# Kernel tuning notes

Hardware: AMD Instinct MI355X
Metric: run time of the kernel (lower is better)

## Reference

```python
import jax, jax.numpy as jnp
import numpy as np

# dims: B=32 batch, F=40 max_frames, NB=36 num_boxes, R=512 region size, H=512 hidden
# feat_size D = R + 2H = 1536 ; relation attn input = 2D = 3072

def _soft_attention(feats, hidden, Wf, bf, Wh, bh, wa):
    # feats: (N, L, Din), hidden: (N, H) -> att feat (N, Din), alpha (N, L)
    e = jnp.tanh(feats @ Wf.T + bf + (hidden @ Wh.T + bh)[:, None, :]) @ wa  # (N, L)
    alpha = jax.nn.softmax(e, axis=1)
    att = jnp.einsum('nl,nld->nd', alpha, feats)
    return att, alpha


def setup_inputs() -> dict:
    key = jax.random.key(0)
    ks = jax.random.split(key, 16)
    B, F, NB, R, H = 32, 40, 36, 512, 512
    D = R + 2 * H  # 1536
    s = 0.02
    inp = {
        'i3d_feats': jax.random.normal(ks[0], (B, F, 2 * H), jnp.float32),
        'object_feats': jax.random.normal(ks[1], (B, F, NB, R), jnp.float32),
        'hidden_state': jax.random.normal(ks[2], (B, H), jnp.float32),
        # spatial SoftAttention(R, H, H)
        'Ws_f': jax.random.normal(ks[3], (H, R), jnp.float32) * s,
        'bs_f': jnp.zeros((H,), jnp.float32),
        'Ws_h': jax.random.normal(ks[4], (H, H), jnp.float32) * s,
        'bs_h': jnp.zeros((H,), jnp.float32),
        'was': jax.random.normal(ks[5], (H,), jnp.float32) * s,
        # relation SoftAttention(2D, H, H)
        'Wr_f': jax.random.normal(ks[6], (H, 2 * D), jnp.float32) * s,
        'br_f': jnp.zeros((H,), jnp.float32),
        'Wr_h': jax.random.normal(ks[7], (H, H), jnp.float32) * s,
        'br_h': jnp.zeros((H,), jnp.float32),
        'war': jax.random.normal(ks[8], (H,), jnp.float32) * s,
    }
    return inp


def reference(i3d_feats, object_feats, hidden_state,
              Ws_f, bs_f, Ws_h, bs_h, was,
              Wr_f, br_f, Wr_h, br_h, war):
    B, F, NB, R = object_feats.shape
    # ---- spatial attention over boxes (per frame) ----
    feats = object_feats.reshape(B * F, NB, R)
    hidden_rep = jnp.repeat(hidden_state, F, axis=0)  # == hidden.repeat(1,F).reshape(B*F,-1)
    obj_att, _ = _soft_attention(feats, hidden_rep, Ws_f, bs_f, Ws_h, bs_h, was)
    obj_att = obj_att.reshape(B, F, R)
    feat = jnp.concatenate([obj_att, i3d_feats], axis=-1)  # (B, F, D)
    D = feat.shape[-1]
    # ---- relation attention over all F*F frame pairs ----
    # pairwise[b, i*F + j] = concat(feat[b, j], feat[b, i])  (feat1 varies fast, feat2 slow)
    # Decompose Wr_f @ concat(fj, fi) = Wr1 @ fj + Wr2 @ fi to avoid O(F^2 * 2D) tensor.
    Wr1, Wr2 = Wr_f[:, :D], Wr_f[:, D:]
    p1 = feat @ Wr1.T  # (B, F, H), applied to fast index j
    p2 = feat @ Wr2.T  # (B, F, H), applied to slow index i
    hproj = hidden_state @ Wr_h.T + br_h  # (B, H)
    e = jnp.tanh(p2[:, :, None, :] + p1[:, None, :, :] + (hproj + br_f)[:, None, None, :]) @ war  # (B,F,F) [i,j]
    alpha = jax.nn.softmax(e.reshape(B, F * F), axis=1).reshape(B, F, F)
    # weighted sum of concat(feat[j], feat[i]) splits into two marginal sums
    rel1 = jnp.einsum('bij,bjd->bd', alpha, feat)
    rel2 = jnp.einsum('bij,bid->bd', alpha, feat)
    return jnp.concatenate([rel1, rel2], axis=-1)  # (B, 2D)
```

## Files before the change

kernel.cpp:

```cpp
#include <hip/hip_runtime.h>
#include <stdint.h>

#define B_SZ 32
#define F_SZ 40
#define NB_SZ 36
#define R_SZ 512
#define H_SZ 512
#define D_SZ 1536
#define M1 (B_SZ * F_SZ * NB_SZ)
#define NROW (B_SZ * F_SZ)
#define FNB (F_SZ * NB_SZ)

typedef __attribute__((ext_vector_type(8))) short short8;
typedef __attribute__((ext_vector_type(4))) float f32x4;

__device__ __forceinline__ unsigned short f2bf(float f) {
    unsigned int x = __float_as_uint(f);
    return (unsigned short)((x + 0x7fffu + ((x >> 16) & 1u)) >> 16);
}
__device__ __forceinline__ float bf2f(unsigned short u) {
    union { unsigned int i; float f; } v; v.i = ((unsigned int)u) << 16; return v.f;
}
__device__ __forceinline__ unsigned int cvtpk(float lo, float hi) {
    unsigned int r;
    asm("v_cvt_pk_bf16_f32 %0, %1, %2" : "=v"(r) : "v"(lo), "v"(hi));
    return r;
}
__device__ __forceinline__ float fast_rcp(float x) {
    float r; asm("v_rcp_f32 %0, %1" : "=v"(r) : "v"(x)); return r;
}
__device__ __forceinline__ float fast_tanh(float x) {
    float t = __builtin_amdgcn_exp2f(2.8853900817779268f * x);
    return 1.0f - 2.0f * fast_rcp(t + 1.0f);
}

__device__ __forceinline__ void gload_lds16(const void* gsrc, void* ldst) {
    __builtin_amdgcn_global_load_lds(
        (const __attribute__((address_space(1))) unsigned int*)gsrc,
        (__attribute__((address_space(3))) unsigned int*)ldst, 16, 0, 0);
}

__global__ __launch_bounds__(256) void k_pre(
    const float* __restrict__ hidden,
    const float* __restrict__ Wsh, const float* __restrict__ bsh,
    const float* __restrict__ bsf,
    const float* __restrict__ Wrh, const float* __restrict__ brh,
    const float* __restrict__ brf,
    float* __restrict__ hs, float* __restrict__ hr,
    const float* __restrict__ Wsf, unsigned short* __restrict__ Wsb)
{
    const int t = threadIdx.x;
    if (blockIdx.x >= 256) {
        int i = ((blockIdx.x - 256) * 256 + t) * 8;
        float4 f0 = *(const float4*)(Wsf + i);
        float4 f1 = *(const float4*)(Wsf + i + 4);
        uint4 pk = {cvtpk(f0.x, f0.y), cvtpk(f0.z, f0.w),
                    cvtpk(f1.x, f1.y), cvtpk(f1.z, f1.w)};
        *(uint4*)(Wsb + i) = pk;
        return;
    }
    __shared__ float hid[H_SZ];
    const int b = blockIdx.x >> 3, hc = blockIdx.x & 7;
    for (int i = t; i < H_SZ; i += 256) hid[i] = hidden[b * H_SZ + i];
    __syncthreads();
    const int h = hc * 64 + (t >> 2), kq = t & 3;
    const float* r1 = Wsh + (size_t)h * H_SZ + kq * 128;
    const float* r2 = Wrh + (size_t)h * H_SZ + kq * 128;
    const float* hh = hid + kq * 128;
    float a1 = 0.f, a2 = 0.f;
    for (int k = 0; k < 128; k += 4) {
        float4 v1 = *(const float4*)(r1 + k);
        float4 v2 = *(const float4*)(r2 + k);
        a1 += hh[k] * v1.x + hh[k+1] * v1.y + hh[k+2] * v1.z + hh[k+3] * v1.w;
        a2 += hh[k] * v2.x + hh[k+1] * v2.y + hh[k+2] * v2.z + hh[k+3] * v2.w;
    }
    a1 += __shfl_xor(a1, 1); a1 += __shfl_xor(a1, 2);
    a2 += __shfl_xor(a2, 1); a2 += __shfl_xor(a2, 2);
    if (kq == 0) {
        hs[b * H_SZ + h] = a1 + bsh[h] + bsf[h];
        hr[b * H_SZ + h] = a2 + brh[h] + brf[h];
    }
}

__global__ __launch_bounds__(256, 3) void k_e1_mfma(
    const float* __restrict__ feats,
    const unsigned short* __restrict__ Wsb,
    const float* __restrict__ was,
    const float* __restrict__ hs,
    float* __restrict__ e1p)
{
    __shared__ __align__(16) unsigned char As[2][64 * 128];
    __shared__ __align__(16) unsigned char Bs[2][128 * 128];
    __shared__ float hsl[2][256];
    __shared__ float wasl[256];
    __shared__ float eps[2][64];

    const int bx = blockIdx.x;
    const int wid = (bx & 7) * 180 + (bx >> 3);
    const int mb = wid >> 1, by = wid & 1;
    const int m0 = mb * 64, hb = by * 256;
    const int t = threadIdx.x;
    const int b0 = m0 / FNB, b1 = (m0 + 63) / FNB;
    const int thr = (b0 + 1) * FNB - m0;

    if (t < 256) {
        hsl[0][t] = hs[b0 * H_SZ + hb + t];
        hsl[1][t] = hs[b1 * H_SZ + hb + t];
        wasl[t]   = was[hb + t];
    }

    const int lane = t & 63, w = t >> 6;
    const int wr = w >> 1, wc = w & 1;
    const int l15 = lane & 15, lk = lane >> 4;

    int ar[2], brw[4];
#pragma unroll
    for (int i = 0; i < 2; i++) ar[i] = wr * 32 + i * 16 + l15;
#pragma unroll
    for (int j = 0; j < 4; j++) brw[j] = wc * 64 + j * 16 + l15;

    const int srow = t >> 3;
    const int scol = t & 7;
    const int wub  = (t & 192) * 16;

    float4 alo[2], ahi[2];
    f32x4 acc[2][8] = {};
    float ep[2][4] = {{0.f}};

#define E1_LOAD_A(K0) do { \
    _Pragma("unroll") \
    for (int it = 0; it < 2; it++) { \
        int cid = it * 256 + t; \
        int r = cid >> 3, c = cid & 7; \
        const float* src = feats + (size_t)(m0 + r) * R_SZ + (K0) + c * 8; \
        alo[it] = *(const float4*)src; \
        ahi[it] = *(const float4*)(src + 4); \
    } } while (0)

#define E1_WRITE_A(AB) do { \
    _Pragma("unroll") \
    for (int it = 0; it < 2; it++) { \
        int cid = it * 256 + t; \
        int r = cid >> 3, c = cid & 7; \
        uint4 pk = {cvtpk(alo[it].x, alo[it].y), cvtpk(alo[it].z, alo[it].w), \
                    cvtpk(ahi[it].x, ahi[it].y), cvtpk(ahi[it].z, ahi[it].w)}; \
        *(uint4*)(&As[AB][r * 128 + ((c ^ (r & 7)) << 4)]) = pk; \
    } } while (0)

#define E1_STAGE_B(BUF, HP, K0) do { \
    _Pragma("unroll") \
    for (int it = 0; it < 4; it++) { \
        int r = it * 32 + srow; \
        int gc = scol ^ (r & 7); \
        gload_lds16(Wsb + (size_t)(hb + (HP) * 128 + r) * R_SZ + (K0) + gc * 8, \
                    &Bs[BUF][it * 4096 + wub]); \
    } } while (0)

#define E1_COMPUTE(HP, BB, AB) do { \
    _Pragma("unroll") \
    for (int ks = 0; ks < 2; ks++) { \
        short8 a[2], bv[4]; \
        int c = ks * 4 + lk; \
        _Pragma("unroll") \
        for (int i = 0; i < 2; i++) \
            a[i] = *(const short8*)(&As[AB][ar[i] * 128 + ((c ^ (ar[i] & 7)) << 4)]); \
        _Pragma("unroll") \
        for (int j = 0; j < 4; j++) \
            bv[j] = *(const short8*)(&Bs[BB][brw[j] * 128 + ((c ^ (brw[j] & 7)) << 4)]); \
        _Pragma("unroll") \
        for (int i = 0; i < 2; i++) \
        _Pragma("unroll") \
        for (int j = 0; j < 4; j++) \
            acc[i][(HP) * 4 + j] = __builtin_amdgcn_mfma_f32_16x16x32_bf16( \
                a[i], bv[j], acc[i][(HP) * 4 + j], 0, 0, 0); \
    } } while (0)

    E1_LOAD_A(0);
    E1_STAGE_B(0, 0, 0);
    E1_WRITE_A(0);
    __syncthreads();

    for (int ki = 0; ki < 8; ki++) {
        const int ab = ki & 1;
        E1_STAGE_B(1, 1, ki * 64);
        if (ki < 7) E1_LOAD_A((ki + 1) * 64);
        E1_COMPUTE(0, 0, ab);
        __syncthreads();
        if (ki < 7) E1_STAGE_B(0, 0, (ki + 1) * 64);
        E1_COMPUTE(1, 1, ab);
        if (ki < 7) E1_WRITE_A(ab ^ 1);
        __syncthreads();
    }

#pragma unroll
    for (int jj = 0; jj < 8; jj++) {
        int hl = (jj >> 2) * 128 + wc * 64 + (jj & 3) * 16 + l15;
        float wv = wasl[hl];
#pragma unroll
        for (int i = 0; i < 2; i++) {
#pragma unroll
            for (int q = 0; q < 4; q++) {
                int r = wr * 32 + i * 16 + lk * 4 + q;
                float hv = hsl[r >= thr ? 1 : 0][hl];
                ep[i][q] += fast_tanh(acc[i][jj][q] + hv) * wv;
            }
        }
    }
#pragma unroll
    for (int i = 0; i < 2; i++)
#pragma unroll
        for (int q = 0; q < 4; q++) {
            float v = ep[i][q];
            v += __shfl_xor(v, 1);
            v += __shfl_xor(v, 2);
            v += __shfl_xor(v, 4);
            v += __shfl_xor(v, 8);
            if (l15 == 0) eps[wc][wr * 32 + i * 16 + lk * 4 + q] = v;
        }
    __syncthreads();
    if (t < 64) e1p[(size_t)by * M1 + m0 + t] = eps[0][t] + eps[1][t];
#undef E1_LOAD_A
#undef E1_WRITE_A
#undef E1_STAGE_B
#undef E1_COMPUTE
}

__global__ __launch_bounds__(256) void k_softatt(
    const float* __restrict__ feats,
    const float* __restrict__ i3d,
    const float* __restrict__ e1p,
    unsigned short* __restrict__ feat)
{
    __shared__ float alpha[2][NB_SZ];
    const int n0 = blockIdx.x * 2;
    const int t = threadIdx.x;
    const int w = t >> 6;

    if (w < 2) {
        const int n = n0 + w, lane = t & 63;
        float v = -1e30f;
        if (lane < NB_SZ) {
            int idx = n * NB_SZ + lane;
            v = e1p[idx] + e1p[M1 + idx];
        }
        float m = v;
#pragma unroll
        for (int off = 32; off; off >>= 1) m = fmaxf(m, __shfl_xor(m, off));
        float ex = (lane < NB_SZ) ? __expf(v - m) : 0.f;
        float ssum = ex;
#pragma unroll
        for (int off = 32; off; off >>= 1) ssum += __shfl_xor(ssum, off);
        if (lane < NB_SZ) alpha[w][lane] = ex / ssum;
    }
    __syncthreads();

    const int g = t >> 7, lc = t & 127;
    const int n = n0 + g;
    float4 a4 = {0.f, 0.f, 0.f, 0.f};
    const float* base = feats + (size_t)n * NB_SZ * R_SZ + lc * 4;
    for (int ll = 0; ll < NB_SZ; ll++) {
        float al = alpha[g][ll];
        float4 pv = *(const float4*)(base + ll * R_SZ);
        a4.x += al * pv.x; a4.y += al * pv.y;
        a4.z += al * pv.z; a4.w += al * pv.w;
    }
    uint2 att = {cvtpk(a4.x, a4.y), cvtpk(a4.z, a4.w)};
    *(uint2*)(feat + (size_t)n * D_SZ + lc * 4) = att;

    const float* ib = i3d + (size_t)n * 1024 + lc * 8;
    float4 iv0 = *(const float4*)ib;
    float4 iv1 = *(const float4*)(ib + 4);
    uint4 pk = {cvtpk(iv0.x, iv0.y), cvtpk(iv0.z, iv0.w),
                cvtpk(iv1.x, iv1.y), cvtpk(iv1.z, iv1.w)};
    *(uint4*)(feat + (size_t)n * D_SZ + 512 + lc * 8) = pk;
}

__global__ __launch_bounds__(256) void k_pgemm_mfma(
    const unsigned short* __restrict__ feat,
    const float* __restrict__ Wrf,
    float* __restrict__ p)
{
    __shared__ __align__(16) unsigned char As[2][32 * 256];
    __shared__ __align__(16) unsigned char Bs[2][32 * 256];

    const int bx = blockIdx.x;
    const int wid = (bx & 7) * 160 + (bx >> 3);
    const int mb = wid % 40, nb = wid / 40;
    const int m0 = mb * 32, j0 = nb * 32;
    const int t = threadIdx.x;

    const int lane = t & 63, w = t >> 6;
    const int wrm = w >> 1, wcn = w & 1;
    const int l15 = lane & 15, lk = lane >> 4;

    const int arow = wrm * 16 + l15;
    const int brow = wcn * 16 + l15;

    const size_t brow_base = (j0 < 512) ? (size_t)j0 * 3072
                                        : ((size_t)(j0 - 512) * 3072 + 1536);

    float4 blo[2], bhi[2];
    f32x4 acc = {};

#define PG_STAGE_A(BUF, K0) do { \
    _Pragma("unroll") \
    for (int it = 0; it < 2; it++) { \
        int cid = it * 256 + t; \
        int r = cid >> 4, c = cid & 15; \
        int gc = c ^ (r & 7); \
        gload_lds16(feat + (size_t)(m0 + r) * D_SZ + (K0) + gc * 8, \
                    &As[BUF][it * 4096 + (t & 192) * 16]); \
    } } while (0)

#define PG_LOAD_B(K0) do { \
    _Pragma("unroll") \
    for (int it = 0; it < 2; it++) { \
        int cid = it * 256 + t; \
        int r = cid >> 4, c = cid & 15; \
        const float* src = Wrf + brow_base + (size_t)r * 3072 + (K0) + c * 8; \
        blo[it] = *(const float4*)src; \
        bhi[it] = *(const float4*)(src + 4); \
    } } while (0)

#define PG_WRITE_B(BUF) do { \
    _Pragma("unroll") \
    for (int it = 0; it < 2; it++) { \
        int cid = it * 256 + t; \
        int r = cid >> 4, c = cid & 15; \
        uint4 pk = {cvtpk(blo[it].x, blo[it].y), cvtpk(blo[it].z, blo[it].w), \
                    cvtpk(bhi[it].x, bhi[it].y), cvtpk(bhi[it].z, bhi[it].w)}; \
        *(uint4*)(&Bs[BUF][r * 256 + ((c ^ (r & 7)) << 4)]) = pk; \
    } } while (0)

#define PG_COMPUTE(BUF) do { \
    _Pragma("unroll") \
    for (int ks = 0; ks < 4; ks++) { \
        int c = ks * 4 + lk; \
        short8 av = *(const short8*)(&As[BUF][arow * 256 + ((c ^ (arow & 7)) << 4)]); \
        short8 bv = *(const short8*)(&Bs[BUF][brow * 256 + ((c ^ (brow & 7)) << 4)]); \
        acc = __builtin_amdgcn_mfma_f32_16x16x32_bf16(av, bv, acc, 0, 0, 0); \
    } } while (0)

    PG_LOAD_B(0);
    PG_STAGE_A(0, 0);
    PG_WRITE_B(0);
    __syncthreads();

#pragma unroll
    for (int ki = 0; ki < 12; ki++) {
        const int cur = ki & 1;
        if (ki < 11) {
            PG_LOAD_B((ki + 1) * 128);
            PG_STAGE_A(cur ^ 1, (ki + 1) * 128);
        }
        PG_COMPUTE(cur);
        if (ki < 11) PG_WRITE_B(cur ^ 1);
        __syncthreads();
    }

#pragma unroll
    for (int q = 0; q < 4; q++) {
        int row = m0 + wrm * 16 + lk * 4 + q;
        int col = j0 + wcn * 16 + l15;
        p[(size_t)row * 1024 + col] = acc[q];
    }
#undef PG_STAGE_A
#undef PG_LOAD_B
#undef PG_WRITE_B
#undef PG_COMPUTE
}

__global__ __launch_bounds__(256) void k_e2(
    const float* __restrict__ p,
    const float* __restrict__ hr,
    const float* __restrict__ war,
    float* __restrict__ e2)
{
    __shared__ float p1l[F_SZ][512];
    const int blk = blockIdx.x;
    const int b = blk / 10, io = blk % 10;
    const int t = threadIdx.x;
    const int w = t >> 6, l = t & 63;

#pragma unroll
    for (int u = 0; u < 10; u++) {
        int cid = u * 256 + t;
        int r = cid >> 6, c = cid & 63;
        const float* src = p + (size_t)(b * F_SZ + r) * 1024 + c * 8;
        *(float4*)&p1l[r][c * 8]     = *(const float4*)src;
        *(float4*)&p1l[r][c * 8 + 4] = *(const float4*)(src + 4);
    }

    const int i = io * 4 + w;
    const int ni = b * F_SZ + i;
    float base[8], warf[8];
    {
        float4 pa = *(const float4*)(p + (size_t)ni * 1024 + 512 + l * 8);
        float4 pb = *(const float4*)(p + (size_t)ni * 1024 + 512 + l * 8 + 4);
        float4 ha = *(const float4*)(hr + b * H_SZ + l * 8);
        float4 hb = *(const float4*)(hr + b * H_SZ + l * 8 + 4);
        base[0] = pa.x + ha.x; base[1] = pa.y + ha.y; base[2] = pa.z + ha.z; base[3] = pa.w + ha.w;
        base[4] = pb.x + hb.x; base[5] = pb.y + hb.y; base[6] = pb.z + hb.z; base[7] = pb.w + hb.w;
        float4 wa = *(const float4*)(war + l * 8);
        float4 wb = *(const float4*)(war + l * 8 + 4);
        warf[0] = wa.x; warf[1] = wa.y; warf[2] = wa.z; warf[3] = wa.w;
        warf[4] = wb.x; warf[5] = wb.y; warf[6] = wb.z; warf[7] = wb.w;
    }
    __syncthreads();

    for (int j = 0; j < F_SZ; j++) {
        const float* r = p1l[j];
        float4 va = *(const float4*)(r + l * 8);
        float4 vb = *(const float4*)(r + l * 8 + 4);
        float pv[8] = {va.x, va.y, va.z, va.w, vb.x, vb.y, vb.z, vb.w};
        float s = 0.f;
#pragma unroll
        for (int u = 0; u < 8; u++) s += fast_tanh(pv[u] + base[u]) * warf[u];
#pragma unroll
        for (int off = 32; off; off >>= 1) s += __shfl_xor(s, off);
        if (l == 0) e2[(size_t)b * 1600 + i * F_SZ + j] = s;
    }
}

__global__ __launch_bounds__(256) void k_out(
    const float* __restrict__ e2,
    const unsigned short* __restrict__ feat,
    float* __restrict__ out)
{
    __shared__ float alpha[1600];
    __shared__ float red[4];
    __shared__ float rs[F_SZ], cs[F_SZ];
    const int b = blockIdx.x >> 1, half = blockIdx.x & 1;
    const int t = threadIdx.x;
    const int w = t >> 6, l = t & 63;

    float lm = -1e30f;
    for (int idx = t; idx < 1600; idx += 256) {
        float v = e2[(size_t)b * 1600 + idx];
        alpha[idx] = v;
        lm = fmaxf(lm, v);
    }
#pragma unroll
    for (int off = 32; off; off >>= 1) lm = fmaxf(lm, __shfl_xor(lm, off));
    if (l == 0) red[w] = lm;
    __syncthreads();
    float M = fmaxf(fmaxf(red[0], red[1]), fmaxf(red[2], red[3]));
    __syncthreads();
    float ls = 0.f;
    for (int idx = t; idx < 1600; idx += 256) {
        float ex = __expf(alpha[idx] - M);
        alpha[idx] = ex;
        ls += ex;
    }
#pragma unroll
    for (int off = 32; off; off >>= 1) ls += __shfl_xor(ls, off);
    if (l == 0) red[w] = ls;
    __syncthreads();
    float inv = 1.f / (red[0] + red[1] + red[2] + red[3]);

    if (t < F_SZ) {
        float s = 0.f;
        for (int j = 0; j < F_SZ; j++) s += alpha[t * F_SZ + j];
        rs[t] = s * inv;
    } else if (t >= 128 && t < 128 + F_SZ) {
        int j = t - 128;
        float s = 0.f;
        for (int i2 = 0; i2 < F_SZ; i2++) s += alpha[i2 * F_SZ + j];
        cs[j] = s * inv;
    }
    __syncthreads();

    const int cb = half * 768;
    float a1[3] = {0.f, 0.f, 0.f};
    float a2[3] = {0.f, 0.f, 0.f};
    for (int r = 0; r < F_SZ; r++) {
        float w1 = cs[r], w2 = rs[r];
        const unsigned short* fr = feat + (size_t)(b * F_SZ + r) * D_SZ + cb;
#pragma unroll
        for (int u = 0; u < 3; u++) {
            float f = bf2f(fr[t + u * 256]);
            a1[u] += w1 * f;
            a2[u] += w2 * f;
        }
    }
#pragma unroll
    for (int u = 0; u < 3; u++) {
        out[(size_t)b * 3072 + cb + t + u * 256]        = a1[u];
        out[(size_t)b * 3072 + 1536 + cb + t + u * 256] = a2[u];
    }
}

extern "C" void kernel_launch(void* const* d_in, const int* in_sizes, int n_in,
                              void* d_out, int out_size, void* d_ws, size_t ws_size,
                              hipStream_t stream) {
    const float* i3d    = (const float*)d_in[0];
    const float* objf   = (const float*)d_in[1];
    const float* hidden = (const float*)d_in[2];
    const float* Wsf    = (const float*)d_in[3];
    const float* bsf    = (const float*)d_in[4];
    const float* Wsh    = (const float*)d_in[5];
    const float* bsh    = (const float*)d_in[6];
    const float* was    = (const float*)d_in[7];
    const float* Wrf    = (const float*)d_in[8];
    const float* brf    = (const float*)d_in[9];
    const float* Wrh    = (const float*)d_in[10];
    const float* brh    = (const float*)d_in[11];
    const float* war    = (const float*)d_in[12];
    float* out = (float*)d_out;

    char* ws = (char*)d_ws;
    float* hs  = (float*)(ws);
    float* hr  = (float*)(ws + 65536);
    float* p   = (float*)(ws + 131072);
    float* e1p = (float*)(ws + 131072);
    unsigned short* Wsb = (unsigned short*)(ws + 4849664);
    float* e2  = (float*)(ws + 5373952);
    unsigned short* feat = (unsigned short*)(ws + 5578752);

    k_pre<<<dim3(384), dim3(256), 0, stream>>>(hidden, Wsh, bsh, bsf, Wrh, brh, brf, hs, hr, Wsf, Wsb);
    k_e1_mfma<<<dim3(1440), dim3(256), 0, stream>>>(objf, Wsb, was, hs, e1p);
    k_softatt<<<dim3(640), dim3(256), 0, stream>>>(objf, i3d, e1p, feat);
    k_pgemm_mfma<<<dim3(1280), dim3(256), 0, stream>>>(feat, Wrf, p);
    k_e2<<<dim3(320), dim3(256), 0, stream>>>(p, hr, war, e2);
    k_out<<<dim3(64), dim3(256), 0, stream>>>(e2, feat, out);
}
```

Baseline: 273.5 us.

## Tune e1 barriers and priority, widen pgemm M tile, split k_out wider

```diff
diff --git a/kernel.cpp b/kernel.cpp
--- a/kernel.cpp
+++ b/kernel.cpp
@@ -103,11 +103,9 @@
     const int b0 = m0 / FNB, b1 = (m0 + 63) / FNB;
     const int thr = (b0 + 1) * FNB - m0;
 
-    if (t < 256) {
-        hsl[0][t] = hs[b0 * H_SZ + hb + t];
-        hsl[1][t] = hs[b1 * H_SZ + hb + t];
-        wasl[t]   = was[hb + t];
-    }
+    hsl[0][t] = hs[b0 * H_SZ + hb + t];
+    hsl[1][t] = hs[b1 * H_SZ + hb + t];
+    wasl[t]   = was[hb + t];
 
     const int lane = t & 63, w = t >> 6;
     const int wr = w >> 1, wc = w & 1;
@@ -157,6 +155,7 @@
     } } while (0)
 
 #define E1_COMPUTE(HP, BB, AB) do { \
+    __builtin_amdgcn_s_setprio(1); \
     _Pragma("unroll") \
     for (int ks = 0; ks < 2; ks++) { \
         short8 a[2], bv[4]; \
@@ -173,23 +172,30 @@
         for (int j = 0; j < 4; j++) \
             acc[i][(HP) * 4 + j] = __builtin_amdgcn_mfma_f32_16x16x32_bf16( \
                 a[i], bv[j], acc[i][(HP) * 4 + j], 0, 0, 0); \
-    } } while (0)
+    } \
+    __builtin_amdgcn_s_setprio(0); \
+    } while (0)
 
     E1_LOAD_A(0);
     E1_STAGE_B(0, 0, 0);
     E1_WRITE_A(0);
-    __syncthreads();
-
+    asm volatile("s_waitcnt vmcnt(0) lgkmcnt(0)\ns_barrier" ::: "memory");
+
+#pragma unroll
     for (int ki = 0; ki < 8; ki++) {
         const int ab = ki & 1;
         E1_STAGE_B(1, 1, ki * 64);
         if (ki < 7) E1_LOAD_A((ki + 1) * 64);
         E1_COMPUTE(0, 0, ab);
-        __syncthreads();
+        if (ki < 7) {
+            asm volatile("s_waitcnt vmcnt(4)\ns_barrier" ::: "memory");
+        } else {
+            asm volatile("s_waitcnt vmcnt(0)\ns_barrier" ::: "memory");
+        }
         if (ki < 7) E1_STAGE_B(0, 0, (ki + 1) * 64);
         E1_COMPUTE(1, 1, ab);
         if (ki < 7) E1_WRITE_A(ab ^ 1);
-        __syncthreads();
+        asm volatile("s_waitcnt vmcnt(0) lgkmcnt(0)\ns_barrier" ::: "memory");
     }
 
 #pragma unroll
@@ -280,31 +286,32 @@
     const float* __restrict__ Wrf,
     float* __restrict__ p)
 {
-    __shared__ __align__(16) unsigned char As[2][32 * 256];
+    __shared__ __align__(16) unsigned char As[2][64 * 256];
     __shared__ __align__(16) unsigned char Bs[2][32 * 256];
 
     const int bx = blockIdx.x;
-    const int wid = (bx & 7) * 160 + (bx >> 3);
-    const int mb = wid % 40, nb = wid / 40;
-    const int m0 = mb * 32, j0 = nb * 32;
+    const int wid = (bx & 7) * 80 + (bx >> 3);
+    const int mb = wid % 20, nb = wid / 20;
+    const int m0 = mb * 64, j0 = nb * 32;
     const int t = threadIdx.x;
 
     const int lane = t & 63, w = t >> 6;
     const int wrm = w >> 1, wcn = w & 1;
     const int l15 = lane & 15, lk = lane >> 4;
 
-    const int arow = wrm * 16 + l15;
+    int arow[2];
+    arow[0] = wrm * 32 + l15; arow[1] = arow[0] + 16;
     const int brow = wcn * 16 + l15;
 
     const size_t brow_base = (j0 < 512) ? (size_t)j0 * 3072
                                         : ((size_t)(j0 - 512) * 3072 + 1536);
 
     float4 blo[2], bhi[2];
-    f32x4 acc = {};
+    f32x4 acc[2] = {};
 
 #define PG_STAGE_A(BUF, K0) do { \
     _Pragma("unroll") \
-    for (int it = 0; it < 2; it++) { \
+    for (int it = 0; it < 4; it++) { \
         int cid = it * 256 + t; \
         int r = cid >> 4, c = cid & 15; \
         int gc = c ^ (r & 7); \
@@ -333,13 +340,18 @@
     } } while (0)
 
 #define PG_COMPUTE(BUF) do { \
+    __builtin_amdgcn_s_setprio(1); \
     _Pragma("unroll") \
     for (int ks = 0; ks < 4; ks++) { \
         int c = ks * 4 + lk; \
-        short8 av = *(const short8*)(&As[BUF][arow * 256 + ((c ^ (arow & 7)) << 4)]); \
+        short8 a0 = *(const short8*)(&As[BUF][arow[0] * 256 + ((c ^ (arow[0] & 7)) << 4)]); \
+        short8 a1 = *(const short8*)(&As[BUF][arow[1] * 256 + ((c ^ (arow[1] & 7)) << 4)]); \
         short8 bv = *(const short8*)(&Bs[BUF][brow * 256 + ((c ^ (brow & 7)) << 4)]); \
-        acc = __builtin_amdgcn_mfma_f32_16x16x32_bf16(av, bv, acc, 0, 0, 0); \
-    } } while (0)
+        acc[0] = __builtin_amdgcn_mfma_f32_16x16x32_bf16(a0, bv, acc[0], 0, 0, 0); \
+        acc[1] = __builtin_amdgcn_mfma_f32_16x16x32_bf16(a1, bv, acc[1], 0, 0, 0); \
+    } \
+    __builtin_amdgcn_s_setprio(0); \
+    } while (0)
 
     PG_LOAD_B(0);
     PG_STAGE_A(0, 0);
@@ -359,11 +371,13 @@
     }
 
 #pragma unroll
-    for (int q = 0; q < 4; q++) {
-        int row = m0 + wrm * 16 + lk * 4 + q;
-        int col = j0 + wcn * 16 + l15;
-        p[(size_t)row * 1024 + col] = acc[q];
-    }
+    for (int i = 0; i < 2; i++)
+#pragma unroll
+        for (int q = 0; q < 4; q++) {
+            int row = m0 + wrm * 32 + i * 16 + lk * 4 + q;
+            int col = j0 + wcn * 16 + l15;
+            p[(size_t)row * 1024 + col] = acc[i][q];
+        }
 #undef PG_STAGE_A
 #undef PG_LOAD_B
 #undef PG_WRITE_B
@@ -430,7 +444,7 @@
     __shared__ float alpha[1600];
     __shared__ float red[4];
     __shared__ float rs[F_SZ], cs[F_SZ];
-    const int b = blockIdx.x >> 1, half = blockIdx.x & 1;
+    const int b = blockIdx.x / 6, sx = blockIdx.x % 6;
     const int t = threadIdx.x;
     const int w = t >> 6, l = t & 63;
 
@@ -470,24 +484,16 @@
     }
     __syncthreads();
 
-    const int cb = half * 768;
-    float a1[3] = {0.f, 0.f, 0.f};
-    float a2[3] = {0.f, 0.f, 0.f};
+    const int cb = sx * 256;
+    float a1 = 0.f, a2 = 0.f;
     for (int r = 0; r < F_SZ; r++) {
         float w1 = cs[r], w2 = rs[r];
-        const unsigned short* fr = feat + (size_t)(b * F_SZ + r) * D_SZ + cb;
-#pragma unroll
-        for (int u = 0; u < 3; u++) {
-            float f = bf2f(fr[t + u * 256]);
-            a1[u] += w1 * f;
-            a2[u] += w2 * f;
-        }
-    }
-#pragma unroll
-    for (int u = 0; u < 3; u++) {
-        out[(size_t)b * 3072 + cb + t + u * 256]        = a1[u];
-        out[(size_t)b * 3072 + 1536 + cb + t + u * 256] = a2[u];
-    }
+        float f = bf2f(feat[(size_t)(b * F_SZ + r) * D_SZ + cb + t]);
+        a1 += w1 * f;
+        a2 += w2 * f;
+    }
+    out[(size_t)b * 3072 + cb + t]        = a1;
+    out[(size_t)b * 3072 + 1536 + cb + t] = a2;
 }
 
 extern "C" void kernel_launch(void* const* d_in, const int* in_sizes, int n_in,
@@ -520,7 +526,7 @@
     k_pre<<<dim3(384), dim3(256), 0, stream>>>(hidden, Wsh, bsh, bsf, Wrh, brh, brf, hs, hr, Wsf, Wsb);
     k_e1_mfma<<<dim3(1440), dim3(256), 0, stream>>>(objf, Wsb, was, hs, e1p);
     k_softatt<<<dim3(640), dim3(256), 0, stream>>>(objf, i3d, e1p, feat);
-    k_pgemm_mfma<<<dim3(1280), dim3(256), 0, stream>>>(feat, Wrf, p);
+    k_pgemm_mfma<<<dim3(640), dim3(256), 0, stream>>>(feat, Wrf, p);
     k_e2<<<dim3(320), dim3(256), 0, stream>>>(p, hr, war, e2);
-    k_out<<<dim3(64), dim3(256), 0, stream>>>(e2, feat, out);
-}
+    k_out<<<dim3(192), dim3(256), 0, stream>>>(e2, feat, out);
+}
```

Result: faster. 262.9 us (-3.9%).
